# Kernel tuning notes

Hardware: AMD Instinct MI355X
Metric: run time of the kernel (lower is better)

## Reference

```python
import jax, jax.numpy as jnp
import numpy as np

# Static config (matches init_kwargs)
B, H, W, C = 32, 56, 56, 512
NH, WS, SH = 16, 7, 3
HD = C // NH            # head dim = 32
WW = WS * WS            # 49 positions per window
PL, PR, PT, PB = WS - SH, SH, WS - SH, SH   # padding 4,3,4,3
_H, _W = H + WS, W + WS  # 63, 63 (padded, divisible by WS)
HID = 4 * C


def layer_norm(x, g, b, eps=1e-5):
    m = x.mean(-1, keepdims=True)
    v = ((x - m) ** 2).mean(-1, keepdims=True)
    return (x - m) / jnp.sqrt(v + eps) * g + b


def setup_inputs() -> dict:
    key = jax.random.key(0)
    ks = jax.random.split(key, 6)
    s = lambda k, shape, sc=0.02: jax.random.normal(k, shape, jnp.float32) * sc
    return {
        "x": jax.random.normal(ks[0], (B, H * W, C), jnp.float32),
        "g1": jnp.ones((C,), jnp.float32), "b1": jnp.zeros((C,), jnp.float32),
        # spatial_mlp = Conv1d(NH*WW, NH*WW, k=1, groups=NH) -> per-head [WW,WW] weight + [WW] bias
        "sw": s(ks[1], (NH, WW, WW), 0.05), "sb": jnp.zeros((NH, WW), jnp.float32),
        "g2": jnp.ones((C,), jnp.float32), "b2": jnp.zeros((C,), jnp.float32),
        "w1": s(ks[2], (C, HID)), "bb1": jnp.zeros((HID,), jnp.float32),
        "w2": s(ks[3], (HID, C)), "bb2": jnp.zeros((C,), jnp.float32),
    }


def reference(x, g1, b1, sw, sb, g2, b2, w1, bb1, w2, bb2):
    shortcut = x
    h = layer_norm(x, g1, b1).reshape(B, H, W, C)
    # shifted padding (shift_size > 0 branch)
    h = jnp.pad(h, ((0, 0), (PT, PB), (PL, PR), (0, 0)))  # [B,_H,_W,C]
    nH, nW = _H // WS, _W // WS
    # window partition -> [nW_B, NH, WW, HD]
    h = (h.reshape(B, nH, WS, nW, WS, C)
          .transpose(0, 1, 3, 2, 4, 5)
          .reshape(B * nH * nW, WW, NH, HD)
          .transpose(0, 2, 1, 3))
    # grouped 1x1 conv == per-head spatial mix over window positions
    h = jnp.einsum('hij,nhjd->nhid', sw, h) + sb[None, :, :, None]
    # window reverse -> [B,_H,_W,C], then crop padding
    h = (h.transpose(0, 2, 1, 3)
          .reshape(B, nH, nW, WS, WS, C)
          .transpose(0, 1, 3, 2, 4, 5)
          .reshape(B, _H, _W, C))
    h = h[:, PT:PT + H, PL:PL + W, :].reshape(B, H * W, C)
    x = shortcut + h
    # MLP with residual
    h2 = layer_norm(x, g2, b2)
    h2 = jax.nn.gelu(h2 @ w1 + bb1, approximate=False) @ w2 + bb2
    return x + h2
```

## Files before the change

### kernel.cpp

```cpp
#include <hip/hip_runtime.h>
#include <cstdint>

using u16 = unsigned short;
using u32 = unsigned int;

typedef __bf16 bf16x8 __attribute__((ext_vector_type(8)));
typedef float f32x4 __attribute__((ext_vector_type(4)));

__device__ __forceinline__ float bf2f(u16 u) {
    u32 v = ((u32)u) << 16; float f; __builtin_memcpy(&f, &v, 4); return f;
}
__device__ __forceinline__ u16 f2bf(float f) {
    u32 u; __builtin_memcpy(&u, &f, 4);
    u32 r = (u + 0x7fffu + ((u >> 16) & 1u)) >> 16; return (u16)r;
}
__device__ __forceinline__ u32 pack2(float a, float b) {
    return (u32)f2bf(a) | ((u32)f2bf(b) << 16);
}
__device__ __forceinline__ int xcd_swz(int orig, int nwg) {
    int q = nwg >> 3, r8 = nwg & 7;
    int xcd = orig & 7, slot = orig >> 3;
    return (xcd < r8 ? xcd * (q + 1) : r8 * (q + 1) + (xcd - r8) * q) + slot;
}
__device__ __forceinline__ void async_cp16(const u16* g, u16* l) {
    __builtin_amdgcn_global_load_lds(
        (const __attribute__((address_space(1))) void*)g,
        (__attribute__((address_space(3))) void*)l, 16, 0, 0);
}

__global__ __launch_bounds__(256) void transp_k(const float* __restrict__ in,
                                                u16* __restrict__ outp,
                                                int R, int C) {
    __shared__ alignas(16) u16 t[32][33];
    int tx = threadIdx.x & 31, ty = threadIdx.x >> 5;
    int bx = blockIdx.x * 32, by = blockIdx.y * 32;
#pragma unroll
    for (int i = 0; i < 4; ++i)
        t[ty + i * 8][tx] = f2bf(in[(size_t)(by + ty + i * 8) * C + bx + tx]);
    __syncthreads();
#pragma unroll
    for (int i = 0; i < 4; ++i)
        outp[(size_t)(bx + ty + i * 8) * R + by + tx] = t[tx][ty + i * 8];
}

__global__ __launch_bounds__(256) void swb_k(const float* __restrict__ sw,
                                             u16* __restrict__ swb) {
    int idx = blockIdx.x * 256 + threadIdx.x;
    int h = idx >> 12, r = (idx >> 6) & 63, j = idx & 63;
    u16 v = 0;
    if (r < 49 && j < 49) v = f2bf(sw[(size_t)h * 2401 + r * 49 + j]);
    swb[idx] = v;
}

__global__ __launch_bounds__(512) void spatial_k(const float* __restrict__ xin,
                                                 const float* __restrict__ g1,
                                                 const float* __restrict__ b1,
                                                 const u16* __restrict__ swb,
                                                 const float* __restrict__ sb,
                                                 const float* __restrict__ g2,
                                                 const float* __restrict__ b2,
                                                 u16* __restrict__ xmid,
                                                 u16* __restrict__ ln2o) {
    __shared__ alignas(16) u16 raw[49 * 512];
    __shared__ alignas(16) u16 lnT[512 * 72];
    __shared__ float sbl[784];
    __shared__ float psumL[64][8], psqL[64][8];
    __shared__ float2 mrs[64];
    __shared__ int toks[49];
    const int tid = threadIdx.x;
    const int wid = blockIdx.x;
    const int b = wid / 81, rem = wid % 81;
    const int wy = rem / 9, wx = rem % 9;

    if (tid < 49) {
        int py = tid / 7, px = tid % 7;
        int y = wy * 7 + py - 4, x = wx * 7 + px - 4;
        toks[tid] = ((unsigned)y < 56u && (unsigned)x < 56u)
                        ? (b * 3136 + y * 56 + x) : -1;
    }
    for (int idx = tid; idx < 784; idx += 512) sbl[idx] = sb[idx];
    __syncthreads();

    const int l = tid & 63, wvi = tid >> 6;
    const int lr = l & 15, lk = l >> 4;

    {
        float g1v[8], b1v[8];
#pragma unroll
        for (int j = 0; j < 8; ++j) { g1v[j] = g1[l * 8 + j]; b1v[j] = b1[l * 8 + j]; }
        for (int p = wvi; p < 49; p += 8) {
            int tk = toks[p];
            uint4 w = make_uint4(0, 0, 0, 0);
            if (tk >= 0) {
                const float4* pp = (const float4*)(xin + (size_t)tk * 512 + l * 8);
                float4 a = pp[0], bb = pp[1];
                float v[8] = {a.x, a.y, a.z, a.w, bb.x, bb.y, bb.z, bb.w};
                float s = 0.f, qq = 0.f;
#pragma unroll
                for (int j = 0; j < 8; ++j) { s += v[j]; qq += v[j] * v[j]; }
#pragma unroll
                for (int off = 1; off < 64; off <<= 1) {
                    s += __shfl_xor(s, off); qq += __shfl_xor(qq, off);
                }
                float m = s * (1.f / 512.f);
                float var = qq * (1.f / 512.f) - m * m;
                float r = rsqrtf(var + 1e-5f);
                float o[8];
#pragma unroll
                for (int j = 0; j < 8; ++j)
                    o[j] = (v[j] - m) * r * g1v[j] + b1v[j];
                w.x = pack2(o[0], o[1]); w.y = pack2(o[2], o[3]);
                w.z = pack2(o[4], o[5]); w.w = pack2(o[6], o[7]);
            }
            *(uint4*)(raw + p * 512 + l * 8) = w;
        }
    }
    __syncthreads();

    {
        const int c = tid;
#pragma unroll
        for (int m = 0; m < 8; ++m) {
            u32 d[4];
#pragma unroll
            for (int e2 = 0; e2 < 4; ++e2) {
                int j0 = m * 8 + e2 * 2, j1 = j0 + 1;
                u16 v0 = (j0 < 49) ? raw[j0 * 512 + c] : (u16)0;
                u16 v1 = (j1 < 49) ? raw[j1 * 512 + c] : (u16)0;
                d[e2] = (u32)v0 | ((u32)v1 << 16);
            }
            uint4 w = make_uint4(d[0], d[1], d[2], d[3]);
            *(uint4*)(lnT + c * 72 + ((m ^ (c & 7)) * 8)) = w;
        }
    }
    __syncthreads();

    f32x4 acc[2][4][2] = {};
#pragma unroll
    for (int hh = 0; hh < 2; ++hh) {
        const int h = wvi * 2 + hh;
        bf16x8 bfr[2][2];
#pragma unroll
        for (int tn = 0; tn < 2; ++tn)
#pragma unroll
            for (int kk = 0; kk < 2; ++kk) {
                int crow = h * 32 + tn * 16 + lr;
                bfr[tn][kk] = *reinterpret_cast<const bf16x8*>(
                    lnT + crow * 72 + (((kk * 4 + lk) ^ (crow & 7)) * 8));
            }
        bf16x8 af[4][2];
#pragma unroll
        for (int tp = 0; tp < 4; ++tp)
#pragma unroll
            for (int kk = 0; kk < 2; ++kk)
                af[tp][kk] = *reinterpret_cast<const bf16x8*>(
                    swb + h * 4096 + (tp * 16 + lr) * 64 + (kk * 4 + lk) * 8);
#pragma unroll
        for (int tp = 0; tp < 4; ++tp)
#pragma unroll
            for (int tn = 0; tn < 2; ++tn)
#pragma unroll
                for (int kk = 0; kk < 2; ++kk)
                    acc[hh][tp][tn] = __builtin_amdgcn_mfma_f32_16x16x32_bf16(
                        af[tp][kk], bfr[tn][kk], acc[hh][tp][tn], 0, 0, 0);
    }

    float g2v[2][2], b2v[2][2];
#pragma unroll
    for (int hh = 0; hh < 2; ++hh)
#pragma unroll
        for (int tn = 0; tn < 2; ++tn) {
            int c = (wvi * 2 + hh) * 32 + tn * 16 + lr;
            g2v[hh][tn] = g2[c]; b2v[hh][tn] = b2[c];
        }

    float sp[4][4], qp[4][4];
#pragma unroll
    for (int tp = 0; tp < 4; ++tp)
#pragma unroll
        for (int rg = 0; rg < 4; ++rg) { sp[tp][rg] = 0.f; qp[tp][rg] = 0.f; }

#pragma unroll
    for (int hh = 0; hh < 2; ++hh) {
        const int h = wvi * 2 + hh;
#pragma unroll
        for (int tp = 0; tp < 4; ++tp)
#pragma unroll
            for (int tn = 0; tn < 2; ++tn)
#pragma unroll
                for (int rg = 0; rg < 4; ++rg) {
                    int p = tp * 16 + lk * 4 + rg;
                    if (p < 49) {
                        int tk = toks[p];
                        if (tk >= 0) {
                            int c = h * 32 + tn * 16 + lr;
                            float o = acc[hh][tp][tn][rg] + sbl[h * 49 + p]
                                      + xin[(size_t)tk * 512 + c];
                            acc[hh][tp][tn][rg] = o;
                            sp[tp][rg] += o;
                            qp[tp][rg] += o * o;
                        }
                    }
                }
    }
#pragma unroll
    for (int tp = 0; tp < 4; ++tp)
#pragma unroll
        for (int rg = 0; rg < 4; ++rg) {
#pragma unroll
            for (int off = 1; off < 16; off <<= 1) {
                sp[tp][rg] += __shfl_xor(sp[tp][rg], off);
                qp[tp][rg] += __shfl_xor(qp[tp][rg], off);
            }
        }
    if (lr == 0) {
#pragma unroll
        for (int tp = 0; tp < 4; ++tp)
#pragma unroll
            for (int rg = 0; rg < 4; ++rg) {
                int p = tp * 16 + lk * 4 + rg;
                psumL[p][wvi] = sp[tp][rg];
                psqL[p][wvi] = qp[tp][rg];
            }
    }
    __syncthreads();
    if (tid < 64) {
        float ts = 0.f, tq = 0.f;
#pragma unroll
        for (int w8 = 0; w8 < 8; ++w8) { ts += psumL[tid][w8]; tq += psqL[tid][w8]; }
        float m = ts * (1.f / 512.f);
        float var = tq * (1.f / 512.f) - m * m;
        mrs[tid] = make_float2(m, rsqrtf(var + 1e-5f));
    }
    __syncthreads();

#pragma unroll
    for (int hh = 0; hh < 2; ++hh) {
        const int h = wvi * 2 + hh;
#pragma unroll
        for (int tp = 0; tp < 4; ++tp)
#pragma unroll
            for (int rg = 0; rg < 4; ++rg) {
                int p = tp * 16 + lk * 4 + rg;
                if (p < 49) {
                    int tk = toks[p];
                    if (tk >= 0) {
                        float2 mr = mrs[p];
#pragma unroll
                        for (int tn = 0; tn < 2; ++tn) {
                            int c = h * 32 + tn * 16 + lr;
                            float o = acc[hh][tp][tn][rg];
                            xmid[(size_t)tk * 512 + c] = f2bf(o);
                            ln2o[(size_t)tk * 512 + c] =
                                f2bf((o - mr.x) * mr.y * g2v[hh][tn] + b2v[hh][tn]);
                        }
                    }
                }
            }
    }
}

template <int KD, int ND, int EPI>
__global__ __launch_bounds__(512) void gemm_k(const u16* __restrict__ A,
                                              const u16* __restrict__ Wt,
                                              const float* __restrict__ bias,
                                              const u16* __restrict__ Xm,
                                              void* __restrict__ Out, int row0) {
    __shared__ alignas(16) u16 smem[2 * 32768];
    const int tid = threadIdx.x;
    const int l = tid & 63, wid = tid >> 6;
    const int wm = wid >> 2, wn = wid & 3;
    const int lr = l & 15, lk = l >> 4;

    const int wg = xcd_swz(blockIdx.x, gridDim.x);
    constexpr int NTN = ND / 256;
    const int bm = wg / NTN, bn = wg % NTN;

    const u16* gA[4]; const u16* gB[4];
    int lofs[4];
#pragma unroll
    for (int i = 0; i < 4; ++i) {
        int s = (wid * 4 + i) * 64 + l;
        int rr = s >> 3, pc = s & 7, cc = pc ^ (rr & 7);
        gA[i] = A  + (size_t)(bm * 256 + rr) * KD + cc * 8;
        gB[i] = Wt + (size_t)(bn * 256 + rr) * KD + cc * 8;
        lofs[i] = (wid * 4 + i) * 512;
    }

    f32x4 acc[8][4] = {};

#pragma unroll
    for (int i = 0; i < 4; ++i) async_cp16(gA[i], smem + lofs[i]);
#pragma unroll
    for (int i = 0; i < 4; ++i) async_cp16(gB[i], smem + 16384 + lofs[i]);
#pragma unroll
    for (int i = 0; i < 4; ++i) { gA[i] += 64; gB[i] += 64; }
    asm volatile("s_waitcnt vmcnt(0)" ::: "memory");
    __syncthreads();

    int cur = 0;
    for (int ks = 0; ks < KD; ks += 64) {
        if (ks + 64 < KD) {
            u16* dst = smem + (cur ^ 1) * 32768;
#pragma unroll
            for (int i = 0; i < 4; ++i) async_cp16(gA[i], dst + lofs[i]);
#pragma unroll
            for (int i = 0; i < 4; ++i) async_cp16(gB[i], dst + 16384 + lofs[i]);
#pragma unroll
            for (int i = 0; i < 4; ++i) { gA[i] += 64; gB[i] += 64; }
        }
        const u16* As = smem + cur * 32768;
        const u16* Bs = As + 16384;
#pragma unroll
        for (int kk = 0; kk < 2; ++kk) {
            bf16x8 af[8], bfr[4];
#pragma unroll
            for (int f = 0; f < 8; ++f) {
                int ra = wm * 128 + f * 16 + lr;
                af[f] = *reinterpret_cast<const bf16x8*>(
                    As + ra * 64 + (((kk * 4 + lk) ^ (ra & 7)) * 8));
            }
#pragma unroll
            for (int f = 0; f < 4; ++f) {
                int rb = wn * 64 + f * 16 + lr;
                bfr[f] = *reinterpret_cast<const bf16x8*>(
                    Bs + rb * 64 + (((kk * 4 + lk) ^ (rb & 7)) * 8));
            }
#pragma unroll
            for (int fi = 0; fi < 8; ++fi)
#pragma unroll
                for (int fj = 0; fj < 4; ++fj)
                    acc[fi][fj] = __builtin_amdgcn_mfma_f32_16x16x32_bf16(
                        af[fi], bfr[fj], acc[fi][fj], 0, 0, 0);
        }
        asm volatile("s_waitcnt vmcnt(0)" ::: "memory");
        __syncthreads();
        cur ^= 1;
    }

    if (EPI == 0) {
        u16* O16 = (u16*)Out;
#pragma unroll
        for (int fi = 0; fi < 8; ++fi) {
#pragma unroll
            for (int fj = 0; fj < 4; ++fj) {
#pragma unroll
                for (int rr = 0; rr < 4; ++rr) {
                    int mrow = bm * 256 + wm * 128 + fi * 16 + lk * 4 + rr;
                    int ncol = bn * 256 + wn * 64 + fj * 16 + lr;
                    float v = acc[fi][fj][rr] + bias[ncol];
                    float u_ = v * (0.7978845608028654f + 0.03567740813636141f * v * v);
                    float ge = v / (1.f + __expf(-2.f * u_));
                    O16[(size_t)mrow * ND + ncol] = f2bf(ge);
                }
            }
        }
    } else {
        float* Of = (float*)Out;
        float* Cs = (float*)smem;
#pragma unroll
        for (int half = 0; half < 2; ++half) {
            if (wm == half) {
#pragma unroll
                for (int fi = 0; fi < 8; ++fi) {
#pragma unroll
                    for (int fj = 0; fj < 4; ++fj) {
                        int col = wn * 64 + fj * 16 + lr;
                        float bcol = bias[bn * 256 + col];
#pragma unroll
                        for (int rr = 0; rr < 4; ++rr) {
                            int row = fi * 16 + lk * 4 + rr;
                            Cs[row * 256 + col] = acc[fi][fj][rr] + bcol;
                        }
                    }
                }
            }
            __syncthreads();
#pragma unroll
            for (int it = 0; it < 8; ++it) {
                int row = it * 16 + (tid >> 5);
                int cf = (tid & 31) * 8;
                float4 c0 = *(const float4*)(Cs + row * 256 + cf);
                float4 c1 = *(const float4*)(Cs + row * 256 + cf + 4);
                size_t go = (size_t)(row0 + bm * 256 + half * 128 + row) * ND
                            + bn * 256 + cf;
                uint4 xm = *(const uint4*)(Xm + go);
                const u16* xp = (const u16*)&xm;
                float4 r0, r1;
                r0.x = bf2f(xp[0]) + c0.x; r0.y = bf2f(xp[1]) + c0.y;
                r0.z = bf2f(xp[2]) + c0.z; r0.w = bf2f(xp[3]) + c0.w;
                r1.x = bf2f(xp[4]) + c1.x; r1.y = bf2f(xp[5]) + c1.y;
                r1.z = bf2f(xp[6]) + c1.z; r1.w = bf2f(xp[7]) + c1.w;
                *(float4*)(Of + go) = r0;
                *(float4*)(Of + go + 4) = r1;
            }
            __syncthreads();
        }
    }
}

extern "C" void kernel_launch(void* const* d_in, const int* in_sizes, int n_in,
                              void* d_out, int out_size, void* d_ws, size_t ws_size,
                              hipStream_t stream) {
    const float* x   = (const float*)d_in[0];
    const float* g1  = (const float*)d_in[1];
    const float* b1  = (const float*)d_in[2];
    const float* sw  = (const float*)d_in[3];
    const float* sb  = (const float*)d_in[4];
    const float* g2  = (const float*)d_in[5];
    const float* b2  = (const float*)d_in[6];
    const float* w1  = (const float*)d_in[7];
    const float* bb1 = (const float*)d_in[8];
    const float* w2  = (const float*)d_in[9];
    const float* bb2 = (const float*)d_in[10];
    float* out = (float*)d_out;

    char* ws = (char*)d_ws;
    u16* w1t = (u16*)ws;
    u16* w2t = (u16*)(ws + 2097152);
    u16* swb = (u16*)(ws + 2u * 2097152);
    size_t tok_bytes = (size_t)100352 * 512 * 2;
    u16* ln2c = (u16*)(ws + 2u * 2097152 + 131072);
    u16* xmid = (u16*)(ws + 2u * 2097152 + 131072 + tok_bytes);
    size_t hidoff = 2u * 2097152 + 131072 + 2u * tok_bytes;
    long avail = (long)ws_size - (long)hidoff;
    long maxT = avail / 524288;
    int chunkT = (int)(maxT < 2 ? 2 : (maxT > 784 ? 784 : maxT));
    chunkT &= ~1;
    u16* hid = (u16*)(ws + hidoff);

    transp_k<<<dim3(64, 16), 256, 0, stream>>>(w1, w1t, 512, 2048);
    transp_k<<<dim3(16, 64), 256, 0, stream>>>(w2, w2t, 2048, 512);
    swb_k<<<256, 256, 0, stream>>>(sw, swb);
    spatial_k<<<2592, 512, 0, stream>>>(x, g1, b1, swb, sb, g2, b2, xmid, ln2c);
    for (int t0 = 0; t0 < 784; t0 += chunkT) {
        int nt = (784 - t0) < chunkT ? (784 - t0) : chunkT;
        int nt2 = nt >> 1;
        gemm_k<512, 2048, 0><<<nt2 * 8, 512, 0, stream>>>(
            ln2c + (size_t)t0 * 128 * 512, w1t, bb1, nullptr, hid, 0);
        gemm_k<2048, 512, 1><<<nt2 * 2, 512, 0, stream>>>(
            hid, w2t, bb2, xmid, out, t0 * 128);
    }
}
```

Measured before the change: 951.3 us.

## Stage spatial-mix output in LDS and do row-wise LN2 with vectorized global I/O

The spatial kernel's epilogue now writes the MFMA accumulators (plus bias) into a padded fp32 LDS tile that aliases the raw/lnT buffers. One wave then processes each token row: it reads 8 contiguous channels per lane, adds the residual with float4 loads, reduces the LayerNorm statistics with a wave shuffle, and writes xmid and ln2o as 16-byte stores. This replaces the scattered 2-byte global stores and scalar residual loads of the MFMA fragment layout, along with the cross-wave partial-sum exchange. In exchange it adds an extra LDS round trip and a barrier, and enlarges the LDS pool to about 124KB.

```diff
diff --git a/kernel.cpp b/kernel.cpp
--- a/kernel.cpp
+++ b/kernel.cpp
@@ -61,12 +61,12 @@
                                                  const float* __restrict__ b2,
                                                  u16* __restrict__ xmid,
                                                  u16* __restrict__ ln2o) {
-    __shared__ alignas(16) u16 raw[49 * 512];
-    __shared__ alignas(16) u16 lnT[512 * 72];
+    __shared__ alignas(16) char poolc[123904];
     __shared__ float sbl[784];
-    __shared__ float psumL[64][8], psqL[64][8];
-    __shared__ float2 mrs[64];
     __shared__ int toks[49];
+    u16* raw = (u16*)poolc;
+    u16* lnT = (u16*)(poolc + 50176);
+    float* oL = (float*)poolc;
     const int tid = threadIdx.x;
     const int wid = blockIdx.x;
     const int b = wid / 81, rem = wid % 81;
@@ -164,21 +164,7 @@
                     acc[hh][tp][tn] = __builtin_amdgcn_mfma_f32_16x16x32_bf16(
                         af[tp][kk], bfr[tn][kk], acc[hh][tp][tn], 0, 0, 0);
     }
-
-    float g2v[2][2], b2v[2][2];
-#pragma unroll
-    for (int hh = 0; hh < 2; ++hh)
-#pragma unroll
-        for (int tn = 0; tn < 2; ++tn) {
-            int c = (wvi * 2 + hh) * 32 + tn * 16 + lr;
-            g2v[hh][tn] = g2[c]; b2v[hh][tn] = b2[c];
-        }
-
-    float sp[4][4], qp[4][4];
-#pragma unroll
-    for (int tp = 0; tp < 4; ++tp)
-#pragma unroll
-        for (int rg = 0; rg < 4; ++rg) { sp[tp][rg] = 0.f; qp[tp][rg] = 0.f; }
+    __syncthreads();
 
 #pragma unroll
     for (int hh = 0; hh < 2; ++hh) {
@@ -191,72 +177,49 @@
                 for (int rg = 0; rg < 4; ++rg) {
                     int p = tp * 16 + lk * 4 + rg;
                     if (p < 49) {
-                        int tk = toks[p];
-                        if (tk >= 0) {
-                            int c = h * 32 + tn * 16 + lr;
-                            float o = acc[hh][tp][tn][rg] + sbl[h * 49 + p]
-                                      + xin[(size_t)tk * 512 + c];
-                            acc[hh][tp][tn][rg] = o;
-                            sp[tp][rg] += o;
-                            qp[tp][rg] += o * o;
-                        }
+                        int c = h * 32 + tn * 16 + lr;
+                        oL[p * 520 + c] = acc[hh][tp][tn][rg] + sbl[h * 49 + p];
                     }
                 }
     }
-#pragma unroll
-    for (int tp = 0; tp < 4; ++tp)
-#pragma unroll
-        for (int rg = 0; rg < 4; ++rg) {
-#pragma unroll
-            for (int off = 1; off < 16; off <<= 1) {
-                sp[tp][rg] += __shfl_xor(sp[tp][rg], off);
-                qp[tp][rg] += __shfl_xor(qp[tp][rg], off);
-            }
-        }
-    if (lr == 0) {
-#pragma unroll
-        for (int tp = 0; tp < 4; ++tp)
-#pragma unroll
-            for (int rg = 0; rg < 4; ++rg) {
-                int p = tp * 16 + lk * 4 + rg;
-                psumL[p][wvi] = sp[tp][rg];
-                psqL[p][wvi] = qp[tp][rg];
-            }
-    }
-    __syncthreads();
-    if (tid < 64) {
-        float ts = 0.f, tq = 0.f;
-#pragma unroll
-        for (int w8 = 0; w8 < 8; ++w8) { ts += psumL[tid][w8]; tq += psqL[tid][w8]; }
-        float m = ts * (1.f / 512.f);
-        float var = tq * (1.f / 512.f) - m * m;
-        mrs[tid] = make_float2(m, rsqrtf(var + 1e-5f));
-    }
-    __syncthreads();
-
-#pragma unroll
-    for (int hh = 0; hh < 2; ++hh) {
-        const int h = wvi * 2 + hh;
-#pragma unroll
-        for (int tp = 0; tp < 4; ++tp)
-#pragma unroll
-            for (int rg = 0; rg < 4; ++rg) {
-                int p = tp * 16 + lk * 4 + rg;
-                if (p < 49) {
-                    int tk = toks[p];
-                    if (tk >= 0) {
-                        float2 mr = mrs[p];
-#pragma unroll
-                        for (int tn = 0; tn < 2; ++tn) {
-                            int c = h * 32 + tn * 16 + lr;
-                            float o = acc[hh][tp][tn][rg];
-                            xmid[(size_t)tk * 512 + c] = f2bf(o);
-                            ln2o[(size_t)tk * 512 + c] =
-                                f2bf((o - mr.x) * mr.y * g2v[hh][tn] + b2v[hh][tn]);
-                        }
-                    }
-                }
-            }
+    __syncthreads();
+
+    {
+        float g2v[8], b2v[8];
+#pragma unroll
+        for (int j = 0; j < 8; ++j) { g2v[j] = g2[l * 8 + j]; b2v[j] = b2[l * 8 + j]; }
+        for (int p = wvi; p < 49; p += 8) {
+            int tk = toks[p];
+            if (tk < 0) continue;
+            const float* orow = oL + p * 520 + l * 8;
+            float4 oa = *(const float4*)orow;
+            float4 ob = *(const float4*)(orow + 4);
+            const float4* xp4 = (const float4*)(xin + (size_t)tk * 512 + l * 8);
+            float4 xa = xp4[0], xb = xp4[1];
+            float o[8] = {oa.x + xa.x, oa.y + xa.y, oa.z + xa.z, oa.w + xa.w,
+                          ob.x + xb.x, ob.y + xb.y, ob.z + xb.z, ob.w + xb.w};
+            float s = 0.f, qq = 0.f;
+#pragma unroll
+            for (int j = 0; j < 8; ++j) { s += o[j]; qq += o[j] * o[j]; }
+#pragma unroll
+            for (int off = 1; off < 64; off <<= 1) {
+                s += __shfl_xor(s, off); qq += __shfl_xor(qq, off);
+            }
+            float m = s * (1.f / 512.f);
+            float var = qq * (1.f / 512.f) - m * m;
+            float r = rsqrtf(var + 1e-5f);
+            uint4 wx_, wl_;
+            wx_.x = pack2(o[0], o[1]); wx_.y = pack2(o[2], o[3]);
+            wx_.z = pack2(o[4], o[5]); wx_.w = pack2(o[6], o[7]);
+            float ln[8];
+#pragma unroll
+            for (int j = 0; j < 8; ++j)
+                ln[j] = (o[j] - m) * r * g2v[j] + b2v[j];
+            wl_.x = pack2(ln[0], ln[1]); wl_.y = pack2(ln[2], ln[3]);
+            wl_.z = pack2(ln[4], ln[5]); wl_.w = pack2(ln[6], ln[7]);
+            *(uint4*)(xmid + (size_t)tk * 512 + l * 8) = wx_;
+            *(uint4*)(ln2o + (size_t)tk * 512 + l * 8) = wl_;
+        }
     }
 }
 
```

Measured after the change: 857.5 us, median of 2. 1.11x faster.
